# Performance work log

Hardware: AMD Instinct MI355X
Metric: run time of the kernel (lower is better)

## Reference

```python
import jax, jax.numpy as jnp
import numpy as np

B, S, D, H = 4, 2048, 1024, 16
DK = D // H


def setup_inputs() -> dict:
    key = jax.random.key(0)
    ks = jax.random.split(key, 7)
    s = 1.0 / np.sqrt(D)
    return {
        "q": jax.random.normal(ks[0], (B, S, D), jnp.float32),
        "k": jax.random.normal(ks[1], (B, S, D), jnp.float32),
        "v": jax.random.normal(ks[2], (B, S, D), jnp.float32),
        "Wq": jax.random.normal(ks[3], (D, D), jnp.float32) * s,
        "Wk": jax.random.normal(ks[4], (D, D), jnp.float32) * s,
        "Wv": jax.random.normal(ks[5], (D, D), jnp.float32) * s,
        "Wo": jax.random.normal(ks[6], (D, D), jnp.float32) * s,
    }


def _split(x):
    # [B,S,D] -> [B,H,S,DK]
    return x.reshape(B, S, H, DK).transpose(0, 2, 1, 3)


def reference(q, k, v, Wq, Wk, Wv, Wo):
    # Linear projections (nn.Linear with bias=False: x @ W^T)
    qh = _split(q @ Wq.T)
    kh = _split(k @ Wk.T)
    vh = _split(v @ Wv.T)
    scale = 1.0 / jnp.sqrt(jnp.asarray(DK, qh.dtype))
    # attention scores [B,H,S,S]
    attn = jnp.einsum("bhqd,bhkd->bhqk", qh, kh) * scale
    # causal mask: disallow k > q
    causal = jnp.tril(jnp.ones((S, S), dtype=bool))
    attn = jnp.where(causal[None, None], attn, -jnp.inf)
    attn = jax.nn.softmax(attn, axis=-1)  # dropout p=0.0 -> identity
    out = jnp.einsum("bhqk,bhkd->bhqd", attn, vh)
    # combine heads [B,H,S,DK] -> [B,S,D]
    out = out.transpose(0, 2, 1, 3).reshape(B, S, D)
    return out @ Wo.T
```

## Files before the change

kernel.cpp:

```cpp
#include <hip/hip_runtime.h>
#include <math.h>
#include <stdint.h>

#define B_  4
#define S_  2048
#define D_  1024
#define H_  16
#define DK_ 64
#define NR_ (B_ * S_)

typedef _Float16 half8  __attribute__((ext_vector_type(8)));
typedef _Float16 half4  __attribute__((ext_vector_type(4)));
typedef float    floatx4 __attribute__((ext_vector_type(4)));

__global__ __launch_bounds__(256)
void split_f32(const float* __restrict__ src, _Float16* __restrict__ hi,
               _Float16* __restrict__ lo, int n8) {
    const int i = blockIdx.x * 256 + threadIdx.x;
    if (i >= n8) return;
    const float4* s4 = (const float4*)src;
    float4 a = s4[2 * i];
    float4 b = s4[2 * i + 1];
    float f[8] = {a.x, a.y, a.z, a.w, b.x, b.y, b.z, b.w};
    union { half8 v; _Float16 h[8]; } H, L;
    #pragma unroll
    for (int j = 0; j < 8; ++j) {
        _Float16 h = (_Float16)f[j];
        H.h[j] = h;
        L.h[j] = (_Float16)(f[j] - (float)h);
    }
    *(half8*)(hi + (size_t)i * 8) = H.v;
    *(half8*)(lo + (size_t)i * 8) = L.v;
}

#define GBN 128
#define GBM 128
#define GBK 32
#define LDH 40

__global__ __launch_bounds__(256, 3)
void gemm_xwt_mfma(const _Float16* __restrict__ Xh, const _Float16* __restrict__ Xl,
                   const _Float16* __restrict__ Wh, const _Float16* __restrict__ Wl,
                   void* __restrict__ out0, int mode) {
    __shared__ __align__(16) _Float16 Xhi[GBN][LDH];
    __shared__ __align__(16) _Float16 Xlo[GBN][LDH];
    __shared__ __align__(16) _Float16 Whi[GBM][LDH];
    __shared__ __align__(16) _Float16 Wlo[GBM][LDH];
    const int K = D_;

    const int tid  = threadIdx.x;
    const int wave = tid >> 6;
    const int lane = tid & 63;
    const int row16 = lane & 15;
    const int quad  = lane >> 4;
    const int n0 = blockIdx.x * GBN;
    const int m0 = blockIdx.y * GBM;

    const int xrow = tid >> 1;
    const int xc   = (tid & 1) << 4;

    floatx4 acc[2][8];
    const floatx4 zero4 = {0.f, 0.f, 0.f, 0.f};
    #pragma unroll
    for (int i = 0; i < 2; ++i)
        #pragma unroll
        for (int j = 0; j < 8; ++j) acc[i][j] = zero4;

    uint4 xh0, xh1, xl0, xl1, wh0, wh1, wl0, wl1;
    auto load_regs = [&](int k0) {
        const _Float16* ph = Xh + (size_t)(n0 + xrow) * K + k0 + xc;
        const _Float16* pl = Xl + (size_t)(n0 + xrow) * K + k0 + xc;
        xh0 = *(const uint4*)ph;
        xh1 = *(const uint4*)(ph + 8);
        xl0 = *(const uint4*)pl;
        xl1 = *(const uint4*)(pl + 8);
        const _Float16* pwh = Wh + (size_t)(m0 + xrow) * K + k0 + xc;
        const _Float16* pwl = Wl + (size_t)(m0 + xrow) * K + k0 + xc;
        wh0 = *(const uint4*)pwh;
        wh1 = *(const uint4*)(pwh + 8);
        wl0 = *(const uint4*)pwl;
        wl1 = *(const uint4*)(pwl + 8);
    };

    load_regs(0);
    for (int k0 = 0; k0 < K; k0 += GBK) {
        __syncthreads();
        *(uint4*)&Xhi[xrow][xc]     = xh0;
        *(uint4*)&Xhi[xrow][xc + 8] = xh1;
        *(uint4*)&Xlo[xrow][xc]     = xl0;
        *(uint4*)&Xlo[xrow][xc + 8] = xl1;
        *(uint4*)&Whi[xrow][xc]     = wh0;
        *(uint4*)&Whi[xrow][xc + 8] = wh1;
        *(uint4*)&Wlo[xrow][xc]     = wl0;
        *(uint4*)&Wlo[xrow][xc + 8] = wl1;
        __syncthreads();
        if (k0 + GBK < K) load_regs(k0 + GBK);

        half8 a_hi[2], a_lo[2];
        #pragma unroll
        for (int ni = 0; ni < 2; ++ni) {
            const int r = wave * 32 + ni * 16 + row16;
            a_hi[ni] = *(const half8*)&Xhi[r][quad * 8];
            a_lo[ni] = *(const half8*)&Xlo[r][quad * 8];
        }
        #pragma unroll
        for (int mj = 0; mj < 8; ++mj) {
            const int r = mj * 16 + row16;
            half8 b_hi = *(const half8*)&Whi[r][quad * 8];
            half8 b_lo = *(const half8*)&Wlo[r][quad * 8];
            #pragma unroll
            for (int ni = 0; ni < 2; ++ni) {
                acc[ni][mj] = __builtin_amdgcn_mfma_f32_16x16x32_f16(
                    a_hi[ni], b_hi, acc[ni][mj], 0, 0, 0);
                acc[ni][mj] = __builtin_amdgcn_mfma_f32_16x16x32_f16(
                    a_hi[ni], b_lo, acc[ni][mj], 0, 0, 0);
                acc[ni][mj] = __builtin_amdgcn_mfma_f32_16x16x32_f16(
                    a_lo[ni], b_hi, acc[ni][mj], 0, 0, 0);
            }
        }
    }

    #pragma unroll
    for (int ni = 0; ni < 2; ++ni)
        #pragma unroll
        for (int mj = 0; mj < 8; ++mj) {
            if (mode == 2) {
                const int s  = n0 + wave * 32 + ni * 16 + quad * 4;
                const int b  = s >> 11;
                const int sr = s & (S_ - 1);
                const int m  = m0 + mj * 16 + row16;
                const int h  = m >> 6;
                const int dk = m & 63;
                half4 h4;
                #pragma unroll
                for (int r = 0; r < 4; ++r) h4[r] = (_Float16)acc[ni][mj][r];
                *(half4*)((_Float16*)out0 +
                          (((size_t)b * H_ + h) * DK_ + dk) * S_ + sr) = h4;
            } else {
                #pragma unroll
                for (int rg = 0; rg < 4; ++rg) {
                    const int n = n0 + wave * 32 + ni * 16 + quad * 4 + rg;
                    const int m = m0 + mj * 16 + row16;
                    const float v = acc[ni][mj][rg];
                    if (mode == 0) {
                        ((float*)out0)[(size_t)n * D_ + m] = v;
                    } else {
                        const int b  = n >> 11;
                        const int s  = n & (S_ - 1);
                        const int h  = m >> 6;
                        const int dk = m & 63;
                        union { _Float16 h16; uint16_t u; } hi, lo;
                        hi.h16 = (_Float16)v;
                        lo.h16 = (_Float16)(v - (float)hi.h16);
                        uint32_t u = ((uint32_t)lo.u << 16) | (uint32_t)hi.u;
                        ((uint32_t*)out0)[(((size_t)b * H_ + h) * S_ + s) * DK_ + dk] = u;
                    }
                }
            }
        }
}

__global__ __launch_bounds__(256)
void attn_mfma(const uint32_t* __restrict__ Qhl, const uint32_t* __restrict__ Khl,
               const _Float16* __restrict__ Vth,
               _Float16* __restrict__ Ahi, _Float16* __restrict__ Alo) {
    __shared__ __align__(16) _Float16 KhiC[64][64];
    __shared__ __align__(16) _Float16 KloC[64][64];
    __shared__ __align__(16) _Float16 VC[64][64];
    __shared__ __align__(16) _Float16 PCT[4][16][72];

    const int bh = blockIdx.y;
    const int qt = (int)(gridDim.x - 1) - (int)blockIdx.x;
    const int q0 = qt * 64;
    const int tid  = threadIdx.x;
    const int wave = tid >> 6;
    const int lane = tid & 63;
    const int c    = lane & 15;
    const int quad = lane >> 4;

    const uint32_t* Kb = Khl + (size_t)bh * S_ * DK_;
    const _Float16* Vb = Vth + (size_t)bh * DK_ * S_;

    half8 qhi[2], qlo[2];
    {
        const uint32_t* Qrow = Qhl + ((size_t)bh * S_ + q0 + wave * 16 + c) * DK_;
        #pragma unroll
        for (int ks = 0; ks < 2; ++ks) {
            uint32_t u[8];
            *(uint4*)&u[0] = *(const uint4*)(Qrow + ks * 32 + quad * 8);
            *(uint4*)&u[4] = *(const uint4*)(Qrow + ks * 32 + quad * 8 + 4);
            union { half8 v; uint16_t s[8]; } hi, lo;
            #pragma unroll
            for (int j = 0; j < 8; ++j) {
                hi.s[j] = (uint16_t)(u[j] & 0xffffu);
                lo.s[j] = (uint16_t)(u[j] >> 16);
            }
            qhi[ks] = hi.v; qlo[ks] = lo.v;
        }
    }

    floatx4 acc_o[4];
    const floatx4 zero4 = {0.f, 0.f, 0.f, 0.f};
    #pragma unroll
    for (int dt = 0; dt < 4; ++dt) acc_o[dt] = zero4;
    float mrun = -INFINITY, lrun = 0.f;

    const int srow = tid >> 2;
    const int soff = (tid & 3) * 16;
    const int ch0  = (tid & 3) * 2;

    uint4 ku[4];
    uint4 vv[2];
    auto load_tile = [&](int kt) {
        const uint4* ksrc = (const uint4*)(Kb + (size_t)(kt * 64 + srow) * DK_ + soff);
        ku[0] = ksrc[0]; ku[1] = ksrc[1]; ku[2] = ksrc[2]; ku[3] = ksrc[3];
        const uint4* vsrc = (const uint4*)(Vb + (size_t)srow * S_ + kt * 64 + soff);
        vv[0] = vsrc[0]; vv[1] = vsrc[1];
    };
    auto write_tile = [&]() {
        #pragma unroll
        for (int hf = 0; hf < 2; ++hf) {
            const int swz = ((ch0 + hf) ^ (srow & 7)) * 8;
            uint32_t uu[8];
            *(uint4*)&uu[0] = ku[2 * hf];
            *(uint4*)&uu[4] = ku[2 * hf + 1];
            union { half8 v; uint16_t s[8]; } hi, lo;
            #pragma unroll
            for (int j = 0; j < 8; ++j) {
                hi.s[j] = (uint16_t)(uu[j] & 0xffffu);
                lo.s[j] = (uint16_t)(uu[j] >> 16);
            }
            *(half8*)&KhiC[srow][swz] = hi.v;
            *(half8*)&KloC[srow][swz] = lo.v;
            *(uint4*)&VC[srow][swz]   = vv[hf];
        }
    };

    const int qmy = q0 + wave * 16 + c;
    const floatx4 neg4 = {-INFINITY, -INFINITY, -INFINITY, -INFINITY};

    load_tile(0);
    write_tile();

    for (int kt = 0; kt <= qt; ++kt) {
        const int k0 = kt * 64;
        const bool diag = (kt == qt);
        __syncthreads();
        if (kt < qt) load_tile(kt + 1);

        floatx4 sc[4];
        #pragma unroll
        for (int t = 0; t < 4; ++t) {
            if (diag && t > wave) { sc[t] = neg4; continue; }
            floatx4 s4 = zero4;
            const int krow = t * 16 + c;
            #pragma unroll
            for (int ks = 0; ks < 2; ++ks) {
                const int swz = ((ks * 4 + quad) ^ (krow & 7)) * 8;
                half8 kb = *(const half8*)&KhiC[krow][swz];
                half8 kl = *(const half8*)&KloC[krow][swz];
                s4 = __builtin_amdgcn_mfma_f32_16x16x32_f16(kb, qhi[ks], s4, 0, 0, 0);
                s4 = __builtin_amdgcn_mfma_f32_16x16x32_f16(kl, qhi[ks], s4, 0, 0, 0);
                s4 = __builtin_amdgcn_mfma_f32_16x16x32_f16(kb, qlo[ks], s4, 0, 0, 0);
            }
            #pragma unroll
            for (int r = 0; r < 4; ++r) s4[r] *= 0.125f;
            if (diag && t == wave) {
                #pragma unroll
                for (int r = 0; r < 4; ++r) {
                    const int k = k0 + t * 16 + quad * 4 + r;
                    if (k > qmy) s4[r] = -INFINITY;
                }
            }
            sc[t] = s4;
        }

        float mx = -INFINITY;
        #pragma unroll
        for (int t = 0; t < 4; ++t)
            #pragma unroll
            for (int r = 0; r < 4; ++r) mx = fmaxf(mx, sc[t][r]);
        mx = fmaxf(mx, __shfl_xor(mx, 16));
        mx = fmaxf(mx, __shfl_xor(mx, 32));
        const float mnew  = fmaxf(mrun, mx);
        const float alpha = __expf(mrun - mnew);
        float ls = 0.f;
        #pragma unroll
        for (int t = 0; t < 4; ++t) {
            half4 p4;
            #pragma unroll
            for (int r = 0; r < 4; ++r) {
                const float p = __expf(sc[t][r] - mnew);
                ls += p;
                p4[r] = (_Float16)p;
            }
            *(half4*)&PCT[wave][c][t * 16 + quad * 4] = p4;
        }
        lrun = alpha * lrun + ls;
        mrun = mnew;
        #pragma unroll
        for (int dt = 0; dt < 4; ++dt)
            #pragma unroll
            for (int r = 0; r < 4; ++r) acc_o[dt][r] *= alpha;

        #pragma unroll
        for (int kc = 0; kc < 2; ++kc) {
            if (diag && kc == 1 && wave < 2) continue;
            half8 pb = *(const half8*)&PCT[wave][c][kc * 32 + quad * 8];
            #pragma unroll
            for (int dt = 0; dt < 4; ++dt) {
                const int vrow = dt * 16 + c;
                const int swz = ((kc * 4 + quad) ^ (vrow & 7)) * 8;
                half8 va = *(const half8*)&VC[vrow][swz];
                acc_o[dt] = __builtin_amdgcn_mfma_f32_16x16x32_f16(va, pb, acc_o[dt], 0, 0, 0);
            }
        }

        __syncthreads();
        if (kt < qt) write_tile();
    }

    float l = lrun;
    l += __shfl_xor(l, 16);
    l += __shfl_xor(l, 32);
    const float inv = 1.f / l;
    const int b = bh >> 4, h = bh & 15;
    _Float16* dh = Ahi + ((size_t)b * S_ + qmy) * D_ + h * DK_;
    _Float16* dl = Alo + ((size_t)b * S_ + qmy) * D_ + h * DK_;
    #pragma unroll
    for (int dt = 0; dt < 4; ++dt) {
        half4 hh, ll;
        #pragma unroll
        for (int r = 0; r < 4; ++r) {
            const float o = acc_o[dt][r] * inv;
            hh[r] = (_Float16)o;
            ll[r] = (_Float16)(o - (float)hh[r]);
        }
        *(half4*)(dh + dt * 16 + quad * 4) = hh;
        *(half4*)(dl + dt * 16 + quad * 4) = ll;
    }
}

extern "C" void kernel_launch(void* const* d_in, const int* in_sizes, int n_in,
                              void* d_out, int out_size, void* d_ws, size_t ws_size,
                              hipStream_t stream) {
    const float* q  = (const float*)d_in[0];
    const float* k  = (const float*)d_in[1];
    const float* v  = (const float*)d_in[2];
    const float* Wq = (const float*)d_in[3];
    const float* Wk = (const float*)d_in[4];
    const float* Wv = (const float*)d_in[5];
    const float* Wo = (const float*)d_in[6];
    float* out = (float*)d_out;

    const size_t SZ  = (size_t)B_ * S_ * D_;
    const size_t WSZ = (size_t)D_ * D_;

    _Float16* ws  = (_Float16*)d_ws;
    _Float16* xhi = ws;
    _Float16* xlo = xhi + SZ;
    _Float16* whi = xlo + SZ;
    _Float16* wlo = whi + WSZ;
    uint32_t* Qhl = (uint32_t*)(wlo + WSZ);
    uint32_t* Khl = (uint32_t*)(wlo + WSZ + 2 * SZ);
    _Float16* Vth = wlo + WSZ + 4 * SZ;
    _Float16* Ahi = xhi;
    _Float16* Alo = xlo;

    const int nx8 = (int)(SZ / 8);
    const int nw8 = (int)(WSZ / 8);
    dim3 gb(NR_ / GBN, D_ / GBM);
    dim3 ga(S_ / 64, B_ * H_);

    split_f32<<<nw8 / 256, 256, 0, stream>>>(Wq, whi, wlo, nw8);
    split_f32<<<nx8 / 256, 256, 0, stream>>>(q, xhi, xlo, nx8);
    gemm_xwt_mfma<<<gb, 256, 0, stream>>>(xhi, xlo, whi, wlo, Qhl, 1);

    split_f32<<<nw8 / 256, 256, 0, stream>>>(Wk, whi, wlo, nw8);
    split_f32<<<nx8 / 256, 256, 0, stream>>>(k, xhi, xlo, nx8);
    gemm_xwt_mfma<<<gb, 256, 0, stream>>>(xhi, xlo, whi, wlo, Khl, 1);

    split_f32<<<nw8 / 256, 256, 0, stream>>>(Wv, whi, wlo, nw8);
    split_f32<<<nx8 / 256, 256, 0, stream>>>(v, xhi, xlo, nx8);
    gemm_xwt_mfma<<<gb, 256, 0, stream>>>(xhi, xlo, whi, wlo, Vth, 2);

    attn_mfma<<<ga, 256, 0, stream>>>(Qhl, Khl, Vth, Ahi, Alo);

    split_f32<<<nw8 / 256, 256, 0, stream>>>(Wo, whi, wlo, nw8);
    gemm_xwt_mfma<<<gb, 256, 0, stream>>>(Ahi, Alo, whi, wlo, out, 0);
}
```

Before: 623.0 us.

## Load GEMM A-operand fragments directly from global and batch weight splits

The GEMM now loads the X (activation) MFMA fragments straight from global memory into registers instead of staging them through shared memory, which halves LDS traffic and shared-memory footprint and may raise occupancy. The four weight fp16 hi/lo splits are merged into one launch with separate workspace buffers, removing three kernel launches. The direct loads are strided per lane (16-byte chunks across rows), so global coalescing is worse and depends on L2/L1 reuse.

Result: no change. 616.2 us (-1.1%).

```diff
diff --git a/kernel.cpp b/kernel.cpp
--- a/kernel.cpp
+++ b/kernel.cpp
@@ -33,6 +33,31 @@
     *(half8*)(lo + (size_t)i * 8) = L.v;
 }
 
+__global__ __launch_bounds__(256)
+void split_w4(const float* __restrict__ w0, const float* __restrict__ w1,
+              const float* __restrict__ w2, const float* __restrict__ w3,
+              _Float16* __restrict__ wbase, int n8) {
+    const int i = blockIdx.x * 256 + threadIdx.x;
+    if (i >= n8) return;
+    const float* src = (blockIdx.y == 0) ? w0 : (blockIdx.y == 1) ? w1 :
+                       (blockIdx.y == 2) ? w2 : w3;
+    _Float16* hi = wbase + (size_t)blockIdx.y * 2 * ((size_t)D_ * D_);
+    _Float16* lo = hi + (size_t)D_ * D_;
+    const float4* s4 = (const float4*)src;
+    float4 a = s4[2 * i];
+    float4 b = s4[2 * i + 1];
+    float f[8] = {a.x, a.y, a.z, a.w, b.x, b.y, b.z, b.w};
+    union { half8 v; _Float16 h[8]; } H, L;
+    #pragma unroll
+    for (int j = 0; j < 8; ++j) {
+        _Float16 h = (_Float16)f[j];
+        H.h[j] = h;
+        L.h[j] = (_Float16)(f[j] - (float)h);
+    }
+    *(half8*)(hi + (size_t)i * 8) = H.v;
+    *(half8*)(lo + (size_t)i * 8) = L.v;
+}
+
 #define GBN 128
 #define GBM 128
 #define GBK 32
@@ -42,8 +67,6 @@
 void gemm_xwt_mfma(const _Float16* __restrict__ Xh, const _Float16* __restrict__ Xl,
                    const _Float16* __restrict__ Wh, const _Float16* __restrict__ Wl,
                    void* __restrict__ out0, int mode) {
-    __shared__ __align__(16) _Float16 Xhi[GBN][LDH];
-    __shared__ __align__(16) _Float16 Xlo[GBN][LDH];
     __shared__ __align__(16) _Float16 Whi[GBM][LDH];
     __shared__ __align__(16) _Float16 Wlo[GBM][LDH];
     const int K = D_;
@@ -56,8 +79,11 @@
     const int n0 = blockIdx.x * GBN;
     const int m0 = blockIdx.y * GBM;
 
-    const int xrow = tid >> 1;
-    const int xc   = (tid & 1) << 4;
+    const int wrow = tid >> 1;
+    const int wc   = (tid & 1) << 4;
+
+    const _Float16* aHb = Xh + (size_t)(n0 + wave * 32 + row16) * K + quad * 8;
+    const _Float16* aLb = Xl + (size_t)(n0 + wave * 32 + row16) * K + quad * 8;
 
     floatx4 acc[2][8];
     const floatx4 zero4 = {0.f, 0.f, 0.f, 0.f};
@@ -66,16 +92,15 @@
         #pragma unroll
         for (int j = 0; j < 8; ++j) acc[i][j] = zero4;
 
-    uint4 xh0, xh1, xl0, xl1, wh0, wh1, wl0, wl1;
+    half8 pa_h0, pa_h1, pa_l0, pa_l1;
+    uint4 wh0, wh1, wl0, wl1;
     auto load_regs = [&](int k0) {
-        const _Float16* ph = Xh + (size_t)(n0 + xrow) * K + k0 + xc;
-        const _Float16* pl = Xl + (size_t)(n0 + xrow) * K + k0 + xc;
-        xh0 = *(const uint4*)ph;
-        xh1 = *(const uint4*)(ph + 8);
-        xl0 = *(const uint4*)pl;
-        xl1 = *(const uint4*)(pl + 8);
-        const _Float16* pwh = Wh + (size_t)(m0 + xrow) * K + k0 + xc;
-        const _Float16* pwl = Wl + (size_t)(m0 + xrow) * K + k0 + xc;
+        pa_h0 = *(const half8*)(aHb + k0);
+        pa_h1 = *(const half8*)(aHb + (size_t)16 * K + k0);
+        pa_l0 = *(const half8*)(aLb + k0);
+        pa_l1 = *(const half8*)(aLb + (size_t)16 * K + k0);
+        const _Float16* pwh = Wh + (size_t)(m0 + wrow) * K + k0 + wc;
+        const _Float16* pwl = Wl + (size_t)(m0 + wrow) * K + k0 + wc;
         wh0 = *(const uint4*)pwh;
         wh1 = *(const uint4*)(pwh + 8);
         wl0 = *(const uint4*)pwl;
@@ -84,25 +109,16 @@
 
     load_regs(0);
     for (int k0 = 0; k0 < K; k0 += GBK) {
+        half8 a_hi[2] = {pa_h0, pa_h1};
+        half8 a_lo[2] = {pa_l0, pa_l1};
         __syncthreads();
-        *(uint4*)&Xhi[xrow][xc]     = xh0;
-        *(uint4*)&Xhi[xrow][xc + 8] = xh1;
-        *(uint4*)&Xlo[xrow][xc]     = xl0;
-        *(uint4*)&Xlo[xrow][xc + 8] = xl1;
-        *(uint4*)&Whi[xrow][xc]     = wh0;
-        *(uint4*)&Whi[xrow][xc + 8] = wh1;
-        *(uint4*)&Wlo[xrow][xc]     = wl0;
-        *(uint4*)&Wlo[xrow][xc + 8] = wl1;
+        *(uint4*)&Whi[wrow][wc]     = wh0;
+        *(uint4*)&Whi[wrow][wc + 8] = wh1;
+        *(uint4*)&Wlo[wrow][wc]     = wl0;
+        *(uint4*)&Wlo[wrow][wc + 8] = wl1;
         __syncthreads();
         if (k0 + GBK < K) load_regs(k0 + GBK);
 
-        half8 a_hi[2], a_lo[2];
-        #pragma unroll
-        for (int ni = 0; ni < 2; ++ni) {
-            const int r = wave * 32 + ni * 16 + row16;
-            a_hi[ni] = *(const half8*)&Xhi[r][quad * 8];
-            a_lo[ni] = *(const half8*)&Xlo[r][quad * 8];
-        }
         #pragma unroll
         for (int mj = 0; mj < 8; ++mj) {
             const int r = mj * 16 + row16;
@@ -356,36 +372,39 @@
     const size_t SZ  = (size_t)B_ * S_ * D_;
     const size_t WSZ = (size_t)D_ * D_;
 
-    _Float16* ws  = (_Float16*)d_ws;
-    _Float16* xhi = ws;
-    _Float16* xlo = xhi + SZ;
-    _Float16* whi = xlo + SZ;
-    _Float16* wlo = whi + WSZ;
-    uint32_t* Qhl = (uint32_t*)(wlo + WSZ);
-    uint32_t* Khl = (uint32_t*)(wlo + WSZ + 2 * SZ);
-    _Float16* Vth = wlo + WSZ + 4 * SZ;
+    _Float16* ws    = (_Float16*)d_ws;
+    _Float16* xhi   = ws;
+    _Float16* xlo   = xhi + SZ;
+    _Float16* wbase = xlo + SZ;
+    uint32_t* Qhl = (uint32_t*)(wbase + 8 * WSZ);
+    uint32_t* Khl = (uint32_t*)(wbase + 8 * WSZ + 2 * SZ);
+    _Float16* Vth = wbase + 8 * WSZ + 4 * SZ;
     _Float16* Ahi = xhi;
     _Float16* Alo = xlo;
+
+    _Float16* wq_hi = wbase + 0 * 2 * WSZ, *wq_lo = wq_hi + WSZ;
+    _Float16* wk_hi = wbase + 1 * 2 * WSZ, *wk_lo = wk_hi + WSZ;
+    _Float16* wv_hi = wbase + 2 * 2 * WSZ, *wv_lo = wv_hi + WSZ;
+    _Float16* wo_hi = wbase + 3 * 2 * WSZ, *wo_lo = wo_hi + WSZ;
 
     const int nx8 = (int)(SZ / 8);
     const int nw8 = (int)(WSZ / 8);
     dim3 gb(NR_ / GBN, D_ / GBM);
     dim3 ga(S_ / 64, B_ * H_);
-
-    split_f32<<<nw8 / 256, 256, 0, stream>>>(Wq, whi, wlo, nw8);
+    dim3 gw(nw8 / 256, 4);
+
+    split_w4<<<gw, 256, 0, stream>>>(Wq, Wk, Wv, Wo, wbase, nw8);
+
     split_f32<<<nx8 / 256, 256, 0, stream>>>(q, xhi, xlo, nx8);
-    gemm_xwt_mfma<<<gb, 256, 0, stream>>>(xhi, xlo, whi, wlo, Qhl, 1);
-
-    split_f32<<<nw8 / 256, 256, 0, stream>>>(Wk, whi, wlo, nw8);
+    gemm_xwt_mfma<<<gb, 256, 0, stream>>>(xhi, xlo, wq_hi, wq_lo, Qhl, 1);
+
     split_f32<<<nx8 / 256, 256, 0, stream>>>(k, xhi, xlo, nx8);
-    gemm_xwt_mfma<<<gb, 256, 0, stream>>>(xhi, xlo, whi, wlo, Khl, 1);
-
-    split_f32<<<nw8 / 256, 256, 0, stream>>>(Wv, whi, wlo, nw8);
+    gemm_xwt_mfma<<<gb, 256, 0, stream>>>(xhi, xlo, wk_hi, wk_lo, Khl, 1);
+
     split_f32<<<nx8 / 256, 256, 0, stream>>>(v, xhi, xlo, nx8);
-    gemm_xwt_mfma<<<gb, 256, 0, stream>>>(xhi, xlo, whi, wlo, Vth, 2);
+    gemm_xwt_mfma<<<gb, 256, 0, stream>>>(xhi, xlo, wv_hi, wv_lo, Vth, 2);
 
     attn_mfma<<<ga, 256, 0, stream>>>(Qhl, Khl, Vth, Ahi, Alo);
 
-    split_f32<<<nw8 / 256, 256, 0, stream>>>(Wo, whi, wlo, nw8);
-    gemm_xwt_mfma<<<gb, 256, 0, stream>>>(Ahi, Alo, whi, wlo, out, 0);
+    gemm_xwt_mfma<<<gb, 256, 0, stream>>>(Ahi, Alo, wo_hi, wo_lo, out, 0);
 }
```
